# Performance work log

Measured on AMD Instinct MI355X. Metric: run time of the kernel, lower is better.

The kernel has to match this reference:

```python
import jax, jax.numpy as jnp
import numpy as np

LN_EPS = 1e-5      # torch.nn.LayerNorm default
NORM_EPS = 1e-12   # torch F.normalize default


def _layernorm(x, gamma, beta):
    mu = jnp.mean(x, axis=-1, keepdims=True)
    var = jnp.mean(jnp.square(x - mu), axis=-1, keepdims=True)
    return (x - mu) * jax.lax.rsqrt(var + LN_EPS) * gamma + beta


def _l2norm(x):
    # normalize over last (embedding) axis, matching F.normalize(dim=1) on [B,E,1,N]
    n = jnp.sqrt(jnp.sum(jnp.square(x), axis=-1, keepdims=True))
    return x / jnp.maximum(n, NORM_EPS)


def setup_inputs() -> dict:
    key = jax.random.key(0)
    ks = jax.random.split(key, 4)
    B, N, C, E = 8, 4096, 768, 768
    x = jax.random.normal(ks[0], (B, N, C), dtype=jnp.float32)
    w_qkv = jax.random.normal(ks[1], (C, 3 * E), dtype=jnp.float32) * (1.0 / np.sqrt(C))
    w_proj = jax.random.normal(ks[2], (E, C), dtype=jnp.float32) * (1.0 / np.sqrt(E))
    ln_in_g = jnp.ones((C,), jnp.float32)
    ln_in_b = jnp.zeros((C,), jnp.float32)
    ln_out_g = jnp.ones((E,), jnp.float32)
    ln_out_b = jnp.zeros((E,), jnp.float32)
    return {"x": x, "w_qkv": w_qkv, "w_proj": w_proj,
            "ln_in_g": ln_in_g, "ln_in_b": ln_in_b,
            "ln_out_g": ln_out_g, "ln_out_b": ln_out_b}


def reference(x, w_qkv, w_proj, ln_in_g, ln_in_b, ln_out_g, ln_out_b):
    # x: [B, N, C]
    h = _layernorm(x, ln_in_g, ln_in_b)
    qkv = h @ w_qkv                                  # [B, N, 3E]
    q, k, v = jnp.split(qkv, 3, axis=-1)             # each [B, N, E]
    phi_q = _l2norm(q)                               # per-token L2 over E
    phi_k = _l2norm(k)
    kv = jnp.sum(phi_k * v, axis=1)                  # [B, E] (sum over tokens N)
    attn = phi_q * kv[:, None, :]                    # [B, N, E]
    out = _layernorm(attn, ln_out_g, ln_out_b) @ w_proj  # [B, N, C]
    return out
```

## Files before the change

kernel.cpp:

```cpp
#include <hip/hip_runtime.h>
#include <hip/hip_bf16.h>
#include <cstdint>

typedef __bf16 bf16;
typedef __bf16 bf16x4 __attribute__((ext_vector_type(4)));
typedef __bf16 bf16x8 __attribute__((ext_vector_type(8)));
typedef float f32x4 __attribute__((ext_vector_type(4)));

#define GK 768
#define LN_EPS 1e-5f
#define NORM_EPS 1e-12f

__device__ __forceinline__ void gl_lds16(const void* g, void* l) {
  __builtin_amdgcn_global_load_lds(
      (__attribute__((address_space(1))) uint32_t*)(uintptr_t)g,
      (__attribute__((address_space(3))) uint32_t*)(uintptr_t)l,
      16, 0, 0);
}

__global__ __launch_bounds__(256) void transpose_cvt2(const float* __restrict__ wq,
                                                      const float* __restrict__ wp,
                                                      bf16* __restrict__ wqt,
                                                      bf16* __restrict__ wpt) {
  __shared__ float tile[32][33];
  int bid = blockIdx.x;
  const float* w; bf16* wt; int Ncols, bx, by;
  if (bid < 1728) { w = wq; wt = wqt; Ncols = 2304; bx = bid % 72; by = bid / 72; }
  else { int b2 = bid - 1728; w = wp; wt = wpt; Ncols = 768; bx = b2 % 24; by = b2 / 24; }
  int tx = threadIdx.x & 31, ty = threadIdx.x >> 5;
  int c0 = bx * 32, r0 = by * 32;
  #pragma unroll
  for (int i = 0; i < 32; i += 8)
    tile[ty + i][tx] = w[(size_t)(r0 + ty + i) * Ncols + (c0 + tx)];
  __syncthreads();
  #pragma unroll
  for (int i = 0; i < 32; i += 8)
    wt[(size_t)(c0 + ty + i) * 768 + (r0 + tx)] = (bf16)tile[tx][ty + i];
}

__global__ __launch_bounds__(256) void ln_in_kernel(const float* __restrict__ x,
                                                    const float* __restrict__ g,
                                                    const float* __restrict__ b,
                                                    bf16* __restrict__ h) {
  int wave = threadIdx.x >> 6, lane = threadIdx.x & 63;
  int row = blockIdx.x * 4 + wave;
  const float* xr = x + (size_t)row * 768;
  float4 v0 = ((const float4*)xr)[lane];
  float4 v1 = ((const float4*)xr)[lane + 64];
  float4 v2 = ((const float4*)xr)[lane + 128];
  float s  = v0.x + v0.y + v0.z + v0.w + v1.x + v1.y + v1.z + v1.w
           + v2.x + v2.y + v2.z + v2.w;
  float ss = v0.x*v0.x + v0.y*v0.y + v0.z*v0.z + v0.w*v0.w
           + v1.x*v1.x + v1.y*v1.y + v1.z*v1.z + v1.w*v1.w
           + v2.x*v2.x + v2.y*v2.y + v2.z*v2.z + v2.w*v2.w;
  #pragma unroll
  for (int o = 32; o > 0; o >>= 1) {
    s  += __shfl_xor(s, o, 64);
    ss += __shfl_xor(ss, o, 64);
  }
  float mu  = s * (1.0f / 768.0f);
  float inv = rsqrtf(ss * (1.0f / 768.0f) - mu * mu + LN_EPS);
  bf16* hr = h + (size_t)row * 768;
  #pragma unroll
  for (int c = 0; c < 3; ++c) {
    float4 v = c == 0 ? v0 : (c == 1 ? v1 : v2);
    float4 gg = ((const float4*)g)[lane + c * 64];
    float4 bb = ((const float4*)b)[lane + c * 64];
    bf16x4 o;
    o[0] = (bf16)((v.x - mu) * inv * gg.x + bb.x);
    o[1] = (bf16)((v.y - mu) * inv * gg.y + bb.y);
    o[2] = (bf16)((v.z - mu) * inv * gg.z + bb.z);
    o[3] = (bf16)((v.w - mu) * inv * gg.w + bb.w);
    ((bf16x4*)hr)[lane + c * 64] = o;
  }
}


#define SWZ(x) ((x) ^ ((((x) >> 7) & 7) << 4))

#define BAR __builtin_amdgcn_s_barrier()
#define VMC(n) asm volatile("s_waitcnt vmcnt(" #n ")" ::: "memory")
#define PRIO1 __builtin_amdgcn_s_setprio(1)
#define PRIO0 __builtin_amdgcn_s_setprio(0)

#define LDA1(base, i, ks) \
  af[i][ks] = *(const bf16x8*)((base) + SWZ((wm * 64 + (i) * 16 + llo) * 128 + (ks) * 64 + lhi * 16))
#define LDB1(base, j, ks) \
  bf[j][ks] = *(const bf16x8*)((base) + SWZ((wn * 64 + (j) * 16 + llo) * 128 + (ks) * 64 + lhi * 16))
#define RDALL(Ab, Bb) do { \
  LDA1(Ab, 0, 0); LDA1(Ab, 1, 0); LDA1(Ab, 2, 0); LDA1(Ab, 3, 0); \
  LDB1(Bb, 0, 0); LDB1(Bb, 1, 0); LDB1(Bb, 2, 0); LDB1(Bb, 3, 0); \
  LDA1(Ab, 0, 1); LDA1(Ab, 1, 1); LDA1(Ab, 2, 1); LDA1(Ab, 3, 1); \
  LDB1(Bb, 0, 1); LDB1(Bb, 1, 1); LDB1(Bb, 2, 1); LDB1(Bb, 3, 1); } while (0)

#define MF1(m, n, ks) \
  acc[m][n] = __builtin_amdgcn_mfma_f32_16x16x32_bf16(af[m][ks], bf[n][ks], acc[m][n], 0, 0, 0)
#define MFALL do { PRIO1; \
  MF1(0,0,0); MF1(0,1,0); MF1(0,2,0); MF1(0,3,0); \
  MF1(1,0,0); MF1(1,1,0); MF1(1,2,0); MF1(1,3,0); \
  MF1(2,0,0); MF1(2,1,0); MF1(2,2,0); MF1(2,3,0); \
  MF1(3,0,0); MF1(3,1,0); MF1(3,2,0); MF1(3,3,0); \
  MF1(0,0,1); MF1(0,1,1); MF1(0,2,1); MF1(0,3,1); \
  MF1(1,0,1); MF1(1,1,1); MF1(1,2,1); MF1(1,3,1); \
  MF1(2,0,1); MF1(2,1,1); MF1(2,2,1); MF1(2,3,1); \
  MF1(3,0,1); MF1(3,1,1); MF1(3,2,1); MF1(3,3,1); \
  PRIO0; } while (0)

#define STA2(b, q, t) gl_lds16(A + srcA[q] + (t) * 64, &As_[b][(q) * 2048 + wave * 512])
#define STB2(b, q, t) gl_lds16(Bt + srcB[q] + (t) * 64, &Bs_[b][(q) * 2048 + wave * 512])
#define STAGE(b, t) do { \
  STA2(b, 0, t); STA2(b, 1, t); STA2(b, 2, t); STA2(b, 3, t); \
  STB2(b, 0, t); STB2(b, 1, t); STB2(b, 2, t); STB2(b, 3, t); } while (0)

template <bool OUT_BF16>
__global__ __launch_bounds__(256, 2) void gemm128(const bf16* __restrict__ A,
                                                  const bf16* __restrict__ Bt,
                                                  void* __restrict__ Cv,
                                                  int Nn, int NBN) {
  __shared__ __align__(16) bf16 As_[2][8192];
  __shared__ __align__(16) bf16 Bs_[2][8192];
  const int tid = threadIdx.x;
  const int wave = tid >> 6, lane = tid & 63;
  const int llo = lane & 15, lhi = lane >> 4;
  const int wm = wave >> 1, wn = wave & 1;

  const int nwg = gridDim.x, bid = blockIdx.x;
  const int wg = (bid & 7) * (nwg >> 3) + (bid >> 3);
  const int rb = wg / NBN, cb = wg - rb * NBN;
  const int brow = rb * 128, bcol = cb * 128;

  uint32_t srcA[4], srcB[4];
  #pragma unroll
  for (int q = 0; q < 4; ++q) {
    int d = q * 4096 + tid * 16;
    int a = SWZ(d);
    int r = a >> 7, c = (a & 127) >> 1;
    srcA[q] = (uint32_t)(brow + r) * GK + c;
    srcB[q] = (uint32_t)(bcol + r) * GK + c;
  }

  f32x4 acc[4][4];
  #pragma unroll
  for (int m = 0; m < 4; ++m)
    #pragma unroll
    for (int n = 0; n < 4; ++n) acc[m][n] = (f32x4){0.f, 0.f, 0.f, 0.f};

  bf16x8 af[4][2], bf[4][2];
  const char* As0 = (const char*)&As_[0][0];
  const char* As1 = (const char*)&As_[1][0];
  const char* Bs0 = (const char*)&Bs_[0][0];
  const char* Bs1 = (const char*)&Bs_[1][0];

  STAGE(0, 0);
  STAGE(1, 1);
  VMC(8);
  BAR;

  #pragma unroll
  for (int j = 0; j < 5; ++j) {
    RDALL(As0, Bs0);
    MFALL;
    BAR;
    STAGE(0, 2 * j + 2);
    VMC(8);
    BAR;
    RDALL(As1, Bs1);
    MFALL;
    BAR;
    STAGE(1, 2 * j + 3);
    VMC(8);
    BAR;
  }
  RDALL(As0, Bs0);
  MFALL;
  BAR;
  VMC(0);
  BAR;
  RDALL(As1, Bs1);
  MFALL;

  #pragma unroll
  for (int m = 0; m < 4; ++m) {
    #pragma unroll
    for (int n = 0; n < 4; ++n) {
      int row = brow + wm * 64 + m * 16 + lhi * 4;
      int col = bcol + wn * 64 + n * 16 + llo;
      #pragma unroll
      for (int r2 = 0; r2 < 4; ++r2) {
        if (OUT_BF16)
          ((bf16*)Cv)[(size_t)(row + r2) * Nn + col] = (bf16)acc[m][n][r2];
        else
          ((float*)Cv)[(size_t)(row + r2) * Nn + col] = acc[m][n][r2];
      }
    }
  }
}

__global__ __launch_bounds__(256) void kv_partial(const bf16* __restrict__ qkv,
                                                  float* __restrict__ kvp) {
  __shared__ float sm[4][768];
  int b = blockIdx.x >> 7, chunk = blockIdx.x & 127;
  int wave = threadIdx.x >> 6, lane = threadIdx.x & 63;
  const bf16* base = qkv + ((size_t)(b * 4096 + chunk * 32 + wave * 8)) * 2304;
  float acc8[8] = {}, acc4[4] = {};
  #pragma unroll
  for (int i = 0; i < 8; ++i) {
    const bf16* kr = base + (size_t)i * 2304 + 768;
    const bf16* vr = kr + 768;
    bf16x8 k8 = *(const bf16x8*)(kr + lane * 8);
    bf16x4 k4 = *(const bf16x4*)(kr + 512 + lane * 4);
    bf16x8 v8 = *(const bf16x8*)(vr + lane * 8);
    bf16x4 v4 = *(const bf16x4*)(vr + 512 + lane * 4);
    float kf8[8], kf4[4];
    float ssk = 0.f;
    #pragma unroll
    for (int j = 0; j < 8; ++j) { kf8[j] = (float)k8[j]; ssk += kf8[j] * kf8[j]; }
    #pragma unroll
    for (int j = 0; j < 4; ++j) { kf4[j] = (float)k4[j]; ssk += kf4[j] * kf4[j]; }
    #pragma unroll
    for (int off = 32; off > 0; off >>= 1) ssk += __shfl_xor(ssk, off, 64);
    float wi = 1.0f / fmaxf(sqrtf(ssk), NORM_EPS);
    #pragma unroll
    for (int j = 0; j < 8; ++j) acc8[j] += kf8[j] * (float)v8[j] * wi;
    #pragma unroll
    for (int j = 0; j < 4; ++j) acc4[j] += kf4[j] * (float)v4[j] * wi;
  }
  #pragma unroll
  for (int j = 0; j < 8; ++j) sm[wave][lane * 8 + j] = acc8[j];
  #pragma unroll
  for (int j = 0; j < 4; ++j) sm[wave][512 + lane * 4 + j] = acc4[j];
  __syncthreads();
  int t = threadIdx.x;
  #pragma unroll
  for (int c = 0; c < 3; ++c) {
    int e = c * 256 + t;
    kvp[(size_t)blockIdx.x * 768 + e] = sm[0][e] + sm[1][e] + sm[2][e] + sm[3][e];
  }
}

__global__ __launch_bounds__(256) void kv_reduce(const float* __restrict__ kvp,
                                                 float* __restrict__ kv) {
  int i = blockIdx.x * 256 + threadIdx.x;
  int b = i / 768, e = i - b * 768;
  float s = 0.f;
  #pragma unroll 8
  for (int c = 0; c < 128; ++c) s += kvp[(size_t)(b * 128 + c) * 768 + e];
  kv[i] = s;
}

__global__ __launch_bounds__(256) void attn_ln_kernel(const bf16* __restrict__ qkv,
                                                      const float* __restrict__ kv,
                                                      const float* __restrict__ g,
                                                      const float* __restrict__ b,
                                                      bf16* __restrict__ a) {
  int wave = threadIdx.x >> 6, lane = threadIdx.x & 63;
  int row = blockIdx.x * 4 + wave;
  int bt = row >> 12;
  const bf16* qr = qkv + (size_t)row * 2304;
  bf16x4 q4[3];
  float qf[12];
  float sq = 0.f;
  #pragma unroll
  for (int c = 0; c < 3; ++c) {
    q4[c] = ((const bf16x4*)qr)[lane + c * 64];
    #pragma unroll
    for (int j = 0; j < 4; ++j) {
      float f = (float)q4[c][j];
      qf[c * 4 + j] = f;
      sq += f * f;
    }
  }
  #pragma unroll
  for (int o = 32; o > 0; o >>= 1) sq += __shfl_xor(sq, o, 64);
  float iq = 1.0f / fmaxf(sqrtf(sq), NORM_EPS);
  const float4* kvr = (const float4*)(kv + bt * 768);
  float av[12];
  float s = 0.f, ss = 0.f;
  #pragma unroll
  for (int c = 0; c < 3; ++c) {
    float4 kv4 = kvr[lane + c * 64];
    av[c * 4 + 0] = qf[c * 4 + 0] * iq * kv4.x;
    av[c * 4 + 1] = qf[c * 4 + 1] * iq * kv4.y;
    av[c * 4 + 2] = qf[c * 4 + 2] * iq * kv4.z;
    av[c * 4 + 3] = qf[c * 4 + 3] * iq * kv4.w;
    #pragma unroll
    for (int j = 0; j < 4; ++j) { s += av[c * 4 + j]; ss += av[c * 4 + j] * av[c * 4 + j]; }
  }
  #pragma unroll
  for (int o = 32; o > 0; o >>= 1) {
    s  += __shfl_xor(s, o, 64);
    ss += __shfl_xor(ss, o, 64);
  }
  float mu  = s * (1.0f / 768.0f);
  float inv = rsqrtf(ss * (1.0f / 768.0f) - mu * mu + LN_EPS);
  bf16* ar = a + (size_t)row * 768;
  #pragma unroll
  for (int c = 0; c < 3; ++c) {
    float4 gg = ((const float4*)g)[lane + c * 64];
    float4 bb = ((const float4*)b)[lane + c * 64];
    bf16x4 o;
    o[0] = (bf16)((av[c * 4 + 0] - mu) * inv * gg.x + bb.x);
    o[1] = (bf16)((av[c * 4 + 1] - mu) * inv * gg.y + bb.y);
    o[2] = (bf16)((av[c * 4 + 2] - mu) * inv * gg.z + bb.z);
    o[3] = (bf16)((av[c * 4 + 3] - mu) * inv * gg.w + bb.w);
    ((bf16x4*)ar)[lane + c * 64] = o;
  }
}

extern "C" void kernel_launch(void* const* d_in, const int* in_sizes, int n_in,
                              void* d_out, int out_size, void* d_ws, size_t ws_size,
                              hipStream_t stream) {
  const float* x      = (const float*)d_in[0];
  const float* w_qkv  = (const float*)d_in[1];
  const float* w_proj = (const float*)d_in[2];
  const float* g_in   = (const float*)d_in[3];
  const float* b_in   = (const float*)d_in[4];
  const float* g_out  = (const float*)d_in[5];
  const float* b_out  = (const float*)d_in[6];

  char* ws = (char*)d_ws;
  bf16*  wqkvt  = (bf16*)(ws);
  bf16*  wprojt = (bf16*)(ws + 3538944);
  bf16*  h      = (bf16*)(ws + 4718592);
  bf16*  qkv    = (bf16*)(ws + 55050240);
  float* kvp    = (float*)(ws + 206045184);
  float* kv     = (float*)(ws + 209190912);

  transpose_cvt2<<<2304, 256, 0, stream>>>(w_qkv, w_proj, wqkvt, wprojt);
  ln_in_kernel<<<8192, 256, 0, stream>>>(x, g_in, b_in, h);
  gemm128<true><<<256 * 18, 256, 0, stream>>>(h, wqkvt, (void*)qkv, 2304, 18);
  kv_partial<<<1024, 256, 0, stream>>>(qkv, kvp);
  kv_reduce<<<24, 256, 0, stream>>>(kvp, kv);
  attn_ln_kernel<<<8192, 256, 0, stream>>>(qkv, kv, g_out, b_out, h);
  gemm128<false><<<256 * 6, 256, 0, stream>>>(h, wprojt, d_out, 768, 6);
}
```

Before: 248.4 us.

## Single-buffer GEMM LDS tiles to raise occupancy to four workgroups per CU

Replaces the double-buffered LDS staging in the 128x128 bf16 GEMM with a single buffer and raises launch bounds from 2 to 4 workgroups per CU. LDS per block is halved from 64KB to 32KB, so more workgroups can be resident and hide latency across blocks instead of within one. The cost is that each K step now waits for its global-to-LDS load to finish (vmcnt 0) before compute, removing intra-block overlap, and the higher occupancy target may squeeze registers for the 64-float accumulator.

```diff
diff --git a/kernel.cpp b/kernel.cpp
--- a/kernel.cpp
+++ b/kernel.cpp
@@ -83,15 +83,15 @@
 #define PRIO1 __builtin_amdgcn_s_setprio(1)
 #define PRIO0 __builtin_amdgcn_s_setprio(0)
 
-#define LDA1(base, i, ks) \
-  af[i][ks] = *(const bf16x8*)((base) + SWZ((wm * 64 + (i) * 16 + llo) * 128 + (ks) * 64 + lhi * 16))
-#define LDB1(base, j, ks) \
-  bf[j][ks] = *(const bf16x8*)((base) + SWZ((wn * 64 + (j) * 16 + llo) * 128 + (ks) * 64 + lhi * 16))
-#define RDALL(Ab, Bb) do { \
-  LDA1(Ab, 0, 0); LDA1(Ab, 1, 0); LDA1(Ab, 2, 0); LDA1(Ab, 3, 0); \
-  LDB1(Bb, 0, 0); LDB1(Bb, 1, 0); LDB1(Bb, 2, 0); LDB1(Bb, 3, 0); \
-  LDA1(Ab, 0, 1); LDA1(Ab, 1, 1); LDA1(Ab, 2, 1); LDA1(Ab, 3, 1); \
-  LDB1(Bb, 0, 1); LDB1(Bb, 1, 1); LDB1(Bb, 2, 1); LDB1(Bb, 3, 1); } while (0)
+#define LDA1(i, ks) \
+  af[i][ks] = *(const bf16x8*)(((const char*)As_) + SWZ((wm * 64 + (i) * 16 + llo) * 128 + (ks) * 64 + lhi * 16))
+#define LDB1(j, ks) \
+  bf[j][ks] = *(const bf16x8*)(((const char*)Bs_) + SWZ((wn * 64 + (j) * 16 + llo) * 128 + (ks) * 64 + lhi * 16))
+#define RDALL do { \
+  LDA1(0, 0); LDA1(1, 0); LDA1(2, 0); LDA1(3, 0); \
+  LDB1(0, 0); LDB1(1, 0); LDB1(2, 0); LDB1(3, 0); \
+  LDA1(0, 1); LDA1(1, 1); LDA1(2, 1); LDA1(3, 1); \
+  LDB1(0, 1); LDB1(1, 1); LDB1(2, 1); LDB1(3, 1); } while (0)
 
 #define MF1(m, n, ks) \
   acc[m][n] = __builtin_amdgcn_mfma_f32_16x16x32_bf16(af[m][ks], bf[n][ks], acc[m][n], 0, 0, 0)
@@ -106,19 +106,23 @@
   MF1(3,0,1); MF1(3,1,1); MF1(3,2,1); MF1(3,3,1); \
   PRIO0; } while (0)
 
-#define STA2(b, q, t) gl_lds16(A + srcA[q] + (t) * 64, &As_[b][(q) * 2048 + wave * 512])
-#define STB2(b, q, t) gl_lds16(Bt + srcB[q] + (t) * 64, &Bs_[b][(q) * 2048 + wave * 512])
-#define STAGE(b, t) do { \
-  STA2(b, 0, t); STA2(b, 1, t); STA2(b, 2, t); STA2(b, 3, t); \
-  STB2(b, 0, t); STB2(b, 1, t); STB2(b, 2, t); STB2(b, 3, t); } while (0)
+#define STAGE(t) do { \
+  gl_lds16(A  + srcA[0] + (t) * 64, &As_[0 * 2048 + wave * 512]); \
+  gl_lds16(A  + srcA[1] + (t) * 64, &As_[1 * 2048 + wave * 512]); \
+  gl_lds16(A  + srcA[2] + (t) * 64, &As_[2 * 2048 + wave * 512]); \
+  gl_lds16(A  + srcA[3] + (t) * 64, &As_[3 * 2048 + wave * 512]); \
+  gl_lds16(Bt + srcB[0] + (t) * 64, &Bs_[0 * 2048 + wave * 512]); \
+  gl_lds16(Bt + srcB[1] + (t) * 64, &Bs_[1 * 2048 + wave * 512]); \
+  gl_lds16(Bt + srcB[2] + (t) * 64, &Bs_[2 * 2048 + wave * 512]); \
+  gl_lds16(Bt + srcB[3] + (t) * 64, &Bs_[3 * 2048 + wave * 512]); } while (0)
 
 template <bool OUT_BF16>
-__global__ __launch_bounds__(256, 2) void gemm128(const bf16* __restrict__ A,
+__global__ __launch_bounds__(256, 4) void gemm128(const bf16* __restrict__ A,
                                                   const bf16* __restrict__ Bt,
                                                   void* __restrict__ Cv,
                                                   int Nn, int NBN) {
-  __shared__ __align__(16) bf16 As_[2][8192];
-  __shared__ __align__(16) bf16 Bs_[2][8192];
+  __shared__ __align__(16) bf16 As_[8192];
+  __shared__ __align__(16) bf16 Bs_[8192];
   const int tid = threadIdx.x;
   const int wave = tid >> 6, lane = tid & 63;
   const int llo = lane & 15, lhi = lane >> 4;
@@ -146,38 +150,22 @@
     for (int n = 0; n < 4; ++n) acc[m][n] = (f32x4){0.f, 0.f, 0.f, 0.f};
 
   bf16x8 af[4][2], bf[4][2];
-  const char* As0 = (const char*)&As_[0][0];
-  const char* As1 = (const char*)&As_[1][0];
-  const char* Bs0 = (const char*)&Bs_[0][0];
-  const char* Bs1 = (const char*)&Bs_[1][0];
-
-  STAGE(0, 0);
-  STAGE(1, 1);
-  VMC(8);
-  BAR;
-
-  #pragma unroll
-  for (int j = 0; j < 5; ++j) {
-    RDALL(As0, Bs0);
-    MFALL;
-    BAR;
-    STAGE(0, 2 * j + 2);
-    VMC(8);
-    BAR;
-    RDALL(As1, Bs1);
-    MFALL;
-    BAR;
-    STAGE(1, 2 * j + 3);
-    VMC(8);
-    BAR;
-  }
-  RDALL(As0, Bs0);
-  MFALL;
-  BAR;
+
+  STAGE(0);
   VMC(0);
   BAR;
-  RDALL(As1, Bs1);
-  MFALL;
+
+  #pragma unroll
+  for (int t = 0; t < 12; ++t) {
+    RDALL;
+    MFALL;
+    if (t < 11) {
+      BAR;
+      STAGE(t + 1);
+      VMC(0);
+      BAR;
+    }
+  }
 
   #pragma unroll
   for (int m = 0; m < 4; ++m) {
```

After: 513.5 us. 2.07x slower.
